# Kernel tuning notes

Measured on AMD Instinct MI355X. Metric: run time of the kernel, lower is better.

The kernel has to match this reference:

```python
import jax, jax.numpy as jnp
import numpy as np

N = 50176          # total nodes (128 alternating ligand/protein segments x 392 nodes)
SEGS = 128         # 2*B -> B = 64 complexes
PER = 392
E_BI = N * 4       # covalent-bond graph, avg degree 4
E_KNN = N * 16     # knn spatial graph, avg degree 16
F_IN = 64
D = 128            # f_bond = f_spatial
F_GATHER = 128
N_BOND_STEPS = 2
N_SPATIAL_STEPS = 2

def _lin(k, fi, fo):
    return jax.random.normal(k, (fi, fo), jnp.float32) / np.sqrt(fi)

def setup_inputs():
    ks = iter(jax.random.split(jax.random.key(0), 64))
    inp = {}
    inp["feat"] = jax.random.normal(next(ks), (N, F_IN), jnp.float32)
    inp["bi_src"] = jax.random.randint(next(ks), (E_BI,), 0, N)
    inp["bi_dst"] = jax.random.randint(next(ks), (E_BI,), 0, N)
    inp["bi_etype"] = jax.random.randint(next(ks), (E_BI,), 0, 5)
    inp["knn_src"] = jax.random.randint(next(ks), (E_KNN,), 0, N)
    inp["knn_dst"] = jax.random.randint(next(ks), (E_KNN,), 0, N)
    inp["knn_etype"] = jax.random.randint(next(ks), (E_KNN,), 0, 9)
    inp["batch_num_nodes"] = jnp.full((SEGS,), PER, jnp.int32)
    def gg(prefix, in_f, n_et):
        inp[prefix + "_W"] = jax.random.normal(next(ks), (n_et, D, D), jnp.float32) / np.sqrt(D)
        inp[prefix + "_b"] = jnp.zeros((n_et, D), jnp.float32)
        inp[prefix + "_wih"] = _lin(next(ks), D, 3 * D)
        inp[prefix + "_whh"] = _lin(next(ks), D, 3 * D)
        inp[prefix + "_bih"] = jnp.zeros((3 * D,), jnp.float32)
        inp[prefix + "_bhh"] = jnp.zeros((3 * D,), jnp.float32)
        inp[prefix + "_iw"] = _lin(next(ks), in_f + D, F_GATHER)
        inp[prefix + "_ib"] = jnp.zeros((F_GATHER,), jnp.float32)
        inp[prefix + "_jw"] = _lin(next(ks), D, F_GATHER)
        inp[prefix + "_jb"] = jnp.zeros((F_GATHER,), jnp.float32)
    gg("s1", F_IN, 5)
    gg("s2", F_GATHER, 9)
    inp["s3_w0"] = _lin(next(ks), F_GATHER, 256)
    inp["s3_b0"] = jnp.zeros((256,), jnp.float32)
    inp["s3_w1"] = _lin(next(ks), 256, 128)
    inp["s3_b1"] = jnp.zeros((128,), jnp.float32)
    inp["s3_wo"] = _lin(next(ks), 128, 1)
    inp["s3_bo"] = jnp.zeros((1,), jnp.float32)
    return inp

def _ggc(feat, src, dst, etype, W, b, wih, whh, bih, bhh, iw, ib, jw, jb, n_steps):
    n_nodes = feat.shape[0]
    n_et, d, _ = W.shape
    h = jnp.pad(feat, ((0, 0), (0, d - feat.shape[1])))  # zero_pad to out_feats
    def step(h, _):
        h_src = h[src]  # [E, d] gather
        m = jnp.zeros((src.shape[0], d), h.dtype)
        for i in range(n_et):  # per-edge-type linear, masked by one-hot edge type
            m = m + jnp.where((etype == i)[:, None], h_src @ W[i] + b[i], 0.0)
        a = jax.ops.segment_sum(m, dst, num_segments=n_nodes)  # scatter-sum (fn.sum)
        ir, iz, i_n = jnp.split(a @ wih + bih, 3, axis=-1)     # GRUCell, gate order r,z,n
        hr, hz, hn = jnp.split(h @ whh + bhh, 3, axis=-1)
        r = jax.nn.sigmoid(ir + hr)
        z = jax.nn.sigmoid(iz + hz)
        n = jnp.tanh(i_n + r * hn)
        return (1.0 - z) * n + z * h, None
    h, _ = jax.lax.scan(step, h, None, length=n_steps)
    # dropout is identity in eval mode
    return jax.nn.sigmoid(jnp.concatenate([h, feat], axis=1) @ iw + ib) * (h @ jw + jb)

def reference(feat, bi_src, bi_dst, bi_etype, knn_src, knn_dst, knn_etype, batch_num_nodes,
              s1_W, s1_b, s1_wih, s1_whh, s1_bih, s1_bhh, s1_iw, s1_ib, s1_jw, s1_jb,
              s2_W, s2_b, s2_wih, s2_whh, s2_bih, s2_bhh, s2_iw, s2_ib, s2_jw, s2_jb,
              s3_w0, s3_b0, s3_w1, s3_b1, s3_wo, s3_bo):
    h = _ggc(feat, bi_src, bi_dst, bi_etype, s1_W, s1_b, s1_wih, s1_whh, s1_bih, s1_bhh,
             s1_iw, s1_ib, s1_jw, s1_jb, N_BOND_STEPS)
    h = _ggc(h, knn_src, knn_dst, knn_etype, s2_W, s2_b, s2_wih, s2_whh, s2_bih, s2_bhh,
             s2_iw, s2_ib, s2_jw, s2_jb, N_SPATIAL_STEPS)
    segs = batch_num_nodes.shape[0]
    seg_id = jnp.repeat(jnp.arange(segs), batch_num_nodes, total_repeat_length=h.shape[0])
    pooled = jax.ops.segment_sum(h, seg_id, num_segments=segs)[0::2]  # ligand (even) segments
    x = jax.nn.relu(pooled @ s3_w0 + s3_b0)
    x = jax.nn.relu(x @ s3_w1 + s3_b1)
    return x @ s3_wo + s3_bo
```

## Files before the change

kernel.cpp:

```cpp
#include <hip/hip_runtime.h>
#include <hip/hip_bf16.h>

#define N_NODES 50176
#define PER 392
#define E_BI (N_NODES * 4)
#define E_KNN (N_NODES * 16)
#define E_TOT (E_BI + E_KNN)
#define KN_BI (N_NODES * 5)
#define KN_TOT (N_NODES * 14)
#define AH_S 416
#define AH_U 208

typedef __attribute__((ext_vector_type(8))) short short8;
typedef __attribute__((ext_vector_type(4))) float float4v;
typedef unsigned int uint;
typedef unsigned short ushort;

__device__ __forceinline__ float sigmoidf_(float x) { return 1.f / (1.f + __expf(-x)); }
__device__ __forceinline__ ushort f2bu(float x) {
    __hip_bfloat16 t = __float2bfloat16(x);
    return *reinterpret_cast<ushort*>(&t);
}
__device__ __forceinline__ float blo(uint u) { return __uint_as_float(u << 16); }
__device__ __forceinline__ float bhi(uint u) { return __uint_as_float(u & 0xFFFF0000u); }

__device__ __forceinline__ void gld_lds16(const ushort* g, ushort* l)
{
    __builtin_amdgcn_global_load_lds(
        (const __attribute__((address_space(1))) void*)g,
        (__attribute__((address_space(3))) void*)l, 16, 0, 0);
}

template<int NET>
__global__ __launch_bounds__(256) void msg_kernel(
    const uint* __restrict__ hb,
    const int* __restrict__ indptr,
    const int* __restrict__ elist,
    const ushort* __restrict__ Bfrag,
    ushort* __restrict__ aout)
{
    __shared__ ushort As[4][32][40];
    const int tid = threadIdx.x;
    const int bm = blockIdx.x * 32;
    const int wave = tid >> 6, lane = tid & 63;
    const int quad = lane >> 4, lrow = lane & 15;
    const int wr = wave & 1, wc = wave >> 1;
    const int r = tid >> 3;
    const int oct = tid & 7;
    const int v = bm + r;

    uint* AsU = (uint*)As;

    float4v acc[4] = {};

    for (int et = 0; et < NET; et++) {
        const int beg = indptr[v * NET + et], end = indptr[v * NET + et + 1];
        float av[16];
#pragma unroll
        for (int i = 0; i < 16; i++) av[i] = 0.f;

        for (int j = beg; j < end; j++) {
            int src = elist[j];
            const uint4* hp = (const uint4*)(hb + (size_t)src * 64 + oct * 8);
            uint4 u0 = hp[0];
            uint4 u1 = hp[1];
            av[0] += blo(u0.x); av[1] += bhi(u0.x);
            av[2] += blo(u0.y); av[3] += bhi(u0.y);
            av[4] += blo(u0.z); av[5] += bhi(u0.z);
            av[6] += blo(u0.w); av[7] += bhi(u0.w);
            av[8]  += blo(u1.x); av[9]  += bhi(u1.x);
            av[10] += blo(u1.y); av[11] += bhi(u1.y);
            av[12] += blo(u1.z); av[13] += bhi(u1.z);
            av[14] += blo(u1.w); av[15] += bhi(u1.w);
        }

        __syncthreads();
        {
            int base = ((oct >> 1) * 32 + r) * 20 + (oct & 1) * 8;
#pragma unroll
            for (int u = 0; u < 8; u++)
                AsU[base + u] = (uint)f2bu(av[2 * u]) | ((uint)f2bu(av[2 * u + 1]) << 16);
        }
        __syncthreads();

#pragma unroll
        for (int ch = 0; ch < 4; ch++) {
            short8 af = *(const short8*)&As[ch][wr * 16 + lrow][quad * 8];
            const ushort* bp = Bfrag + ((size_t)(((et * 4 + ch) * 2 + wc) * 4) << 9) + lane * 8;
#pragma unroll
            for (int j2 = 0; j2 < 4; j2++) {
                short8 bfr = *(const short8*)(bp + j2 * 512);
                acc[j2] = __builtin_amdgcn_mfma_f32_16x16x32_bf16(af, bfr, acc[j2], 0, 0, 0);
            }
        }
    }

#pragma unroll
    for (int j2 = 0; j2 < 4; j2++) {
        int col = wc * 64 + j2 * 16 + lrow;
#pragma unroll
        for (int rr = 0; rr < 4; rr++) {
            size_t row = (size_t)(bm + wr * 16 + quad * 4 + rr);
            aout[row * AH_S + col] = f2bu(acc[j2][rr]);
        }
    }
}

__global__ __launch_bounds__(256) void gru_gemm_kernel(
    const ushort* __restrict__ A,
    const ushort* __restrict__ Bt,
    const float* __restrict__ bias,
    ushort* __restrict__ ahOut, ushort* __restrict__ hbS)
{
    __shared__ ushort As[128 * 32];
    __shared__ ushort Bs[128 * 32];
    const int tid = threadIdx.x;
    const int bm = blockIdx.x * 128;
    const int bn = blockIdx.y * 128;
    const int wave = tid >> 6, lane = tid & 63;
    const int quad = lane >> 4, lrow = lane & 15;
    const int wr = wave & 1, wc = wave >> 1;

    float4v acc[4][4] = {};

    for (int k0 = 0; k0 < 288; k0 += 32) {
        __syncthreads();
#pragma unroll
        for (int p = 0; p < 2; p++) {
            int lin = p * 256 + tid;
            int r = lin >> 2;
            int kc = (lin & 3) * 8;
            int wb = (p * 256 + wave * 64) * 8;
            gld_lds16(A + (size_t)(bm + r) * AH_S + k0 + kc, &As[wb]);
            gld_lds16(Bt + (size_t)(bn + r) * 288 + k0 + kc, &Bs[wb]);
        }
        __syncthreads();
        short8 af[4], bfr[4];
#pragma unroll
        for (int i = 0; i < 4; i++)
            af[i] = *(const short8*)&As[(wr * 64 + i * 16 + lrow) * 32 + quad * 8];
#pragma unroll
        for (int j = 0; j < 4; j++)
            bfr[j] = *(const short8*)&Bs[(wc * 64 + j * 16 + lrow) * 32 + quad * 8];
#pragma unroll
        for (int i = 0; i < 4; i++)
#pragma unroll
            for (int j = 0; j < 4; j++)
                acc[i][j] = __builtin_amdgcn_mfma_f32_16x16x32_bf16(af[i], bfr[j], acc[i][j], 0, 0, 0);
    }

    const int ch = (bn >> 7) * 32 + wc * 16 + lrow;
    const float b0 = bias[bn + wc * 64 + lrow];
    const float b1 = bias[bn + wc * 64 + 16 + lrow];
    const float b2 = bias[bn + wc * 64 + 32 + lrow];
    const float b3 = bias[bn + wc * 64 + 48 + lrow];
#pragma unroll
    for (int i = 0; i < 4; i++) {
#pragma unroll
        for (int r = 0; r < 4; r++) {
            size_t row = (size_t)(bm + wr * 64 + i * 16 + quad * 4 + r);
            float rr = sigmoidf_(acc[i][0][r] + b0);
            float zz = sigmoidf_(acc[i][1][r] + b1);
            float nn = tanhf(acc[i][2][r] + b2 + rr * (acc[i][3][r] + b3));
            float hold = __uint_as_float(((uint)A[row * AH_S + 128 + ch]) << 16);
            float hnew = (1.f - zz) * nn + zz * hold;
            ushort hu = f2bu(hnew);
            ahOut[row * AH_S + 128 + ch] = hu;
            hbS[row * 128 + ch] = hu;
        }
    }
}

__global__ __launch_bounds__(256) void ro_gemm_kernel(
    const ushort* __restrict__ A,
    const ushort* __restrict__ Bt,
    const float* __restrict__ bias,
    ushort* __restrict__ rb)
{
    __shared__ ushort As[128 * 32];
    __shared__ ushort Bs[128 * 32];
    const int tid = threadIdx.x;
    const int bm = blockIdx.x * 128;
    const int bn = blockIdx.y * 128;
    const int wave = tid >> 6, lane = tid & 63;
    const int quad = lane >> 4, lrow = lane & 15;
    const int wr = wave & 1, wc = wave >> 1;

    float4v acc[4][4] = {};

    for (int k0 = 0; k0 < 288; k0 += 32) {
        __syncthreads();
#pragma unroll
        for (int p = 0; p < 2; p++) {
            int lin = p * 256 + tid;
            int r = lin >> 2;
            int kc = (lin & 3) * 8;
            int wb = (p * 256 + wave * 64) * 8;
            gld_lds16(A + (size_t)(bm + r) * AH_S + k0 + kc, &As[wb]);
            gld_lds16(Bt + (size_t)(bn + r) * 288 + k0 + kc, &Bs[wb]);
        }
        __syncthreads();
        short8 af[4], bfr[4];
#pragma unroll
        for (int i = 0; i < 4; i++)
            af[i] = *(const short8*)&As[(wr * 64 + i * 16 + lrow) * 32 + quad * 8];
#pragma unroll
        for (int j = 0; j < 4; j++)
            bfr[j] = *(const short8*)&Bs[(wc * 64 + j * 16 + lrow) * 32 + quad * 8];
#pragma unroll
        for (int i = 0; i < 4; i++)
#pragma unroll
            for (int j = 0; j < 4; j++)
                acc[i][j] = __builtin_amdgcn_mfma_f32_16x16x32_bf16(af[i], bfr[j], acc[i][j], 0, 0, 0);
    }

    const int c0 = (bn >> 7) * 64 + wc * 32 + lrow;
    const int c1 = c0 + 16;
    const float bu0 = bias[bn + wc * 64 + lrow];
    const float bv0 = bias[bn + wc * 64 + 16 + lrow];
    const float bu1 = bias[bn + wc * 64 + 32 + lrow];
    const float bv1 = bias[bn + wc * 64 + 48 + lrow];
#pragma unroll
    for (int i = 0; i < 4; i++) {
#pragma unroll
        for (int r = 0; r < 4; r++) {
            size_t row = (size_t)(bm + wr * 64 + i * 16 + quad * 4 + r);
            float o0 = sigmoidf_(acc[i][0][r] + bu0) * (acc[i][1][r] + bv0);
            float o1 = sigmoidf_(acc[i][2][r] + bu1) * (acc[i][3][r] + bv1);
            rb[row * 128 + c0] = f2bu(o0);
            rb[row * 128 + c1] = f2bu(o1);
        }
    }
}

__global__ __launch_bounds__(256) void gemm_kernel(
    const float* __restrict__ A, int lda,
    const float* __restrict__ B, int ldb,
    const float* __restrict__ bias,
    float* __restrict__ C, int ldc,
    int K, int act)
{
    __shared__ float As[32][68];
    __shared__ float Bs[32][68];
    const int tid = threadIdx.x;
    const int bm = blockIdx.x * 64;
    const int bn = blockIdx.y * 64;
    const int tm = (tid & 15) * 4;
    const int tn = (tid >> 4) * 4;
    float acc[4][4] = {};

    for (int k0 = 0; k0 < K; k0 += 32) {
#pragma unroll
        for (int p = 0; p < 2; p++) {
            int lin = p * 256 + tid;
            int ar = lin >> 3;
            int ac = (lin & 7) << 2;
            float4 av = *(const float4*)(A + (size_t)(bm + ar) * lda + (k0 + ac));
            As[ac + 0][ar] = av.x;
            As[ac + 1][ar] = av.y;
            As[ac + 2][ar] = av.z;
            As[ac + 3][ar] = av.w;
            int br = lin >> 4;
            int bc = (lin & 15) << 2;
            *(float4*)&Bs[br][bc] = *(const float4*)(B + (size_t)(k0 + br) * ldb + (bn + bc));
        }
        __syncthreads();
#pragma unroll
        for (int k = 0; k < 32; k++) {
            float4 a4 = *(const float4*)&As[k][tm];
            float4 b4 = *(const float4*)&Bs[k][tn];
            float av[4] = {a4.x, a4.y, a4.z, a4.w};
            float bv[4] = {b4.x, b4.y, b4.z, b4.w};
#pragma unroll
            for (int i = 0; i < 4; i++)
#pragma unroll
                for (int j = 0; j < 4; j++)
                    acc[i][j] += av[i] * bv[j];
        }
        __syncthreads();
    }
#pragma unroll
    for (int i = 0; i < 4; i++) {
        size_t row = (size_t)(bm + tm + i);
#pragma unroll
        for (int j = 0; j < 4; j++) {
            int col = bn + tn + j;
            float val = acc[i][j] + (bias ? bias[col] : 0.f);
            if (act == 1) val = fmaxf(val, 0.f);
            C[row * ldc + col] = val;
        }
    }
}

__global__ void prep_bfrag_kernel(const float* __restrict__ W, __hip_bfloat16* __restrict__ Bf,
                                  int net)
{
    int idx = blockIdx.x * blockDim.x + threadIdx.x;
    int m = idx & 7;
    int lane = (idx >> 3) & 63;
    int f = idx >> 9;
    int j = f & 3; f >>= 2;
    int wc = f & 1; f >>= 1;
    int ch = f & 3;
    int et = f >> 2;
    int quad = lane >> 4, lrow = lane & 15;
    int k = ch * 32 + quad * 8 + m;
    int c = wc * 64 + j * 16 + lrow;
    Bf[idx] = __float2bfloat16(W[et * 16384 + k * 128 + c]);
}

__global__ void prep_gru_kernel(const float* __restrict__ wih, const float* __restrict__ whh,
                                const float* __restrict__ bih, const float* __restrict__ bhh,
                                const float* __restrict__ b, int net,
                                __hip_bfloat16* __restrict__ Bt, float* __restrict__ bias)
{
    int idx = blockIdx.x * blockDim.x + threadIdx.x;
    int p = idx / 288;
    int k = idx - p * 288;
    int g = (p >> 4) & 3;
    int c = (p >> 7) * 32 + ((p >> 6) & 1) * 16 + (p & 15);
    float val = 0.f;
    if (k < 128) {
        if (g == 0)      val = wih[k * 384 + c];
        else if (g == 1) val = wih[k * 384 + 128 + c];
        else if (g == 2) val = wih[k * 384 + 256 + c];
    } else if (k < 256) {
        int kk = k - 128;
        if (g == 0)      val = whh[kk * 384 + c];
        else if (g == 1) val = whh[kk * 384 + 128 + c];
        else if (g == 3) val = whh[kk * 384 + 256 + c];
    } else {
        int j = k - 256;
        if (j < net && g < 3) {
            int col = g * 128 + c;
            float s = 0.f;
            for (int kk = 0; kk < 128; kk++) s += b[j * 128 + kk] * wih[kk * 384 + col];
            val = s;
        }
    }
    Bt[idx] = __float2bfloat16(val);
    if (k == 0) {
        float bv;
        if (g == 0)      bv = bih[c] + bhh[c];
        else if (g == 1) bv = bih[128 + c] + bhh[128 + c];
        else if (g == 2) bv = bih[256 + c];
        else             bv = bhh[256 + c];
        bias[p] = bv;
    }
}

__global__ void prep_ro_kernel(const float* __restrict__ iw, const float* __restrict__ jw,
                               const float* __restrict__ ib, const float* __restrict__ jb,
                               int Fin, __hip_bfloat16* __restrict__ Bt,
                               float* __restrict__ bias)
{
    int idx = blockIdx.x * blockDim.x + threadIdx.x;
    int p = idx / 288;
    int k = idx - p * 288;
    int j = (p >> 4) & 3;
    int s = j & 1;
    int c = ((p >> 7) & 1) * 64 + ((p >> 6) & 1) * 32 + (j >> 1) * 16 + (p & 15);
    float val = 0.f;
    if (k < 128) {
        val = s ? jw[k * 128 + c] : iw[k * 128 + c];
    } else if (k >= 160) {
        int kf = k - 160;
        if (kf < Fin && s == 0) val = iw[(128 + kf) * 128 + c];
    }
    Bt[idx] = __float2bfloat16(val);
    if (k == 0) bias[p] = s ? jb[c] : ib[c];
}

__global__ void hist2_kernel(const int* __restrict__ bd, const int* __restrict__ be,
                             const int* __restrict__ kd, const int* __restrict__ ke,
                             int* __restrict__ counts)
{
    int e = blockIdx.x * blockDim.x + threadIdx.x;
    if (e >= E_TOT) return;
    if (e < E_BI) atomicAdd(&counts[bd[e] * 5 + be[e]], 1);
    else { int i = e - E_BI; atomicAdd(&counts[KN_BI + kd[i] * 9 + ke[i]], 1); }
}

__global__ void scan1_kernel(const int* __restrict__ counts, int* __restrict__ local_ex,
                             int* __restrict__ partial)
{
    __shared__ int s[256];
    int t = threadIdx.x;
    int i = blockIdx.x * 256 + t;
    int v = counts[i];
    s[t] = v;
    __syncthreads();
    for (int off = 1; off < 256; off <<= 1) {
        int x = 0;
        if (t >= off) x = s[t - off];
        __syncthreads();
        if (t >= off) s[t] += x;
        __syncthreads();
    }
    local_ex[i] = s[t] - v;
    if (t == 255) partial[blockIdx.x] = s[255];
}

__global__ void scan2b_kernel(int* __restrict__ partial, int nb, int* __restrict__ last, int E)
{
    __shared__ int s[256];
    int t = threadIdx.x;
    int loc[11];
    int sum = 0;
#pragma unroll
    for (int q = 0; q < 11; q++) {
        int idx = t * 11 + q;
        int v = (idx < nb) ? partial[idx] : 0;
        loc[q] = sum; sum += v;
    }
    s[t] = sum;
    __syncthreads();
    for (int off = 1; off < 256; off <<= 1) {
        int x = 0;
        if (t >= off) x = s[t - off];
        __syncthreads();
        if (t >= off) s[t] += x;
        __syncthreads();
    }
    int excl = s[t] - sum;
#pragma unroll
    for (int q = 0; q < 11; q++) {
        int idx = t * 11 + q;
        if (idx < nb) partial[idx] = excl + loc[q];
    }
    if (t == 0) *last = E;
}

__global__ void scan3c_kernel(int* __restrict__ indptr, const int* __restrict__ partial,
                              int* __restrict__ cursor)
{
    int i = blockIdx.x * 256 + threadIdx.x;
    int v = indptr[i] + partial[blockIdx.x];
    indptr[i] = v;
    cursor[i] = v;
}

__global__ void fill2_kernel(const int* __restrict__ bs, const int* __restrict__ bd,
                             const int* __restrict__ be,
                             const int* __restrict__ ks, const int* __restrict__ kd,
                             const int* __restrict__ ke,
                             int* __restrict__ cursor, int* __restrict__ elist)
{
    int e = blockIdx.x * blockDim.x + threadIdx.x;
    if (e >= E_TOT) return;
    if (e < E_BI) {
        int pos = atomicAdd(&cursor[bd[e] * 5 + be[e]], 1);
        elist[pos] = bs[e];
    } else {
        int i = e - E_BI;
        int pos = atomicAdd(&cursor[KN_BI + kd[i] * 9 + ke[i]], 1);
        elist[pos] = ks[i];
    }
}

__global__ void pad_cnt_kernel(const float* __restrict__ fsrc, const ushort* __restrict__ bsrc,
                               const int* __restrict__ indptr, int net,
                               uint* __restrict__ ahA, uint* __restrict__ ahB,
                               uint* __restrict__ hb, int Fin)
{
    int idx = blockIdx.x * blockDim.x + threadIdx.x;
    int v = idx >> 5;
    int j = idx & 31;
    int c = j * 4;
    float4 val = make_float4(0.f, 0.f, 0.f, 0.f);
    if (bsrc) {
        uint2 u = *(const uint2*)(bsrc + (size_t)v * Fin + c);
        val.x = blo(u.x); val.y = bhi(u.x);
        val.z = blo(u.y); val.w = bhi(u.y);
    } else if (c < Fin) {
        val = *(const float4*)(fsrc + (size_t)v * Fin + c);
    }
    uint2 pk;
    pk.x = (uint)f2bu(val.x) | ((uint)f2bu(val.y) << 16);
    pk.y = (uint)f2bu(val.z) | ((uint)f2bu(val.w) << 16);
    *(uint2*)(ahA + (size_t)v * AH_U + 64 + c / 2) = pk;
    *(uint2*)(ahA + (size_t)v * AH_U + 144 + c / 2) = pk;
    *(uint2*)(ahB + (size_t)v * AH_U + 144 + c / 2) = pk;
    *(uint2*)(hb + (size_t)v * 64 + c / 2) = pk;
    float cv = 0.f;
    if (j < net) cv = (float)(indptr[v * net + j + 1] - indptr[v * net + j]);
    ushort u = f2bu(cv);
    ((ushort*)ahA)[(size_t)v * AH_S + 256 + j] = u;
    ((ushort*)ahB)[(size_t)v * AH_S + 256 + j] = u;
}

__global__ void pool_kernel(const ushort* __restrict__ r2, float* __restrict__ pooled)
{
    int s = blockIdx.x;
    int c = threadIdx.x;
    const ushort* base = r2 + (size_t)(2 * s) * PER * 128;
    float acc = 0.f;
    for (int i = 0; i < PER; i++)
        acc += __uint_as_float(((uint)base[(size_t)i * 128 + c]) << 16);
    pooled[s * 128 + c] = acc;
}

__global__ void out_kernel(const float* __restrict__ x2, const float* __restrict__ wo,
                           const float* __restrict__ bo, float* __restrict__ out)
{
    int row = blockIdx.x;
    int t = threadIdx.x;
    float s = x2[row * 128 + t] * wo[t] + x2[row * 128 + 64 + t] * wo[64 + t];
#pragma unroll
    for (int off = 32; off; off >>= 1) s += __shfl_down(s, off);
    if (t == 0) out[row] = s + bo[0];
}

struct GGParams {
    const float *W, *b, *wih, *whh, *bih, *bhh, *iw, *ib, *jw, *jb;
};

struct WsPtrs {
    __hip_bfloat16 *ah0, *ah1;
    float* G;
    uint* hb;
    __hip_bfloat16* r1b;
    __hip_bfloat16 *bfragB, *gruB, *roB;
    float *gruBias, *roBias;
    int *indptr, *cursor, *partial, *elist;
    float *pooled, *x1, *x2;
};

template<int NET>
static void run_stage(hipStream_t st, const float* featF, const __hip_bfloat16* featB, int Fin,
                      const GGParams& p, const WsPtrs& w, const int* indptr_slice,
                      __hip_bfloat16* rout_b)
{
    const int N = N_NODES;
    ushort* ahA = (ushort*)w.ah0;
    ushort* ahB = (ushort*)w.ah1;
    ushort* hbS = (ushort*)w.hb;

    prep_bfrag_kernel<<<(NET * 16384) / 256, 256, 0, st>>>(p.W, w.bfragB, NET);
    prep_gru_kernel<<<(512 * 288) / 256, 256, 0, st>>>(p.wih, p.whh, p.bih, p.bhh, p.b, NET,
                                                       w.gruB, w.gruBias);
    prep_ro_kernel<<<(256 * 288) / 256, 256, 0, st>>>(p.iw, p.jw, p.ib, p.jb, Fin,
                                                      w.roB, w.roBias);

    pad_cnt_kernel<<<(N * 32) / 256, 256, 0, st>>>(featF, (const ushort*)featB,
                                                   indptr_slice, NET,
                                                   (uint*)ahA, (uint*)ahB, w.hb, Fin);

    ushort* ahIn = ahA;
    ushort* ahOut = ahB;
    for (int step = 0; step < 2; step++) {
        msg_kernel<NET><<<N / 32, 256, 0, st>>>(w.hb, indptr_slice, w.elist,
                                                (ushort*)w.bfragB, ahIn);
        dim3 g(N / 128, 4);
        gru_gemm_kernel<<<g, 256, 0, st>>>(ahIn, (ushort*)w.gruB, w.gruBias, ahOut, hbS);
        ushort* t = ahIn; ahIn = ahOut; ahOut = t;
    }
    dim3 gr(N / 128, 2);
    ro_gemm_kernel<<<gr, 256, 0, st>>>(ahIn + 128, (ushort*)w.roB, w.roBias,
                                       (ushort*)rout_b);
}

extern "C" void kernel_launch(void* const* d_in, const int* in_sizes, int n_in,
                              void* d_out, int out_size, void* d_ws, size_t ws_size,
                              hipStream_t stream)
{
    const float* feat    = (const float*)d_in[0];
    const int*   bi_src  = (const int*)d_in[1];
    const int*   bi_dst  = (const int*)d_in[2];
    const int*   bi_et   = (const int*)d_in[3];
    const int*   knn_src = (const int*)d_in[4];
    const int*   knn_dst = (const int*)d_in[5];
    const int*   knn_et  = (const int*)d_in[6];

    GGParams s1 { (const float*)d_in[8],  (const float*)d_in[9],  (const float*)d_in[10],
                  (const float*)d_in[11], (const float*)d_in[12], (const float*)d_in[13],
                  (const float*)d_in[14], (const float*)d_in[15], (const float*)d_in[16],
                  (const float*)d_in[17] };
    GGParams s2 { (const float*)d_in[18], (const float*)d_in[19], (const float*)d_in[20],
                  (const float*)d_in[21], (const float*)d_in[22], (const float*)d_in[23],
                  (const float*)d_in[24], (const float*)d_in[25], (const float*)d_in[26],
                  (const float*)d_in[27] };
    const float* w0 = (const float*)d_in[28];
    const float* b0 = (const float*)d_in[29];
    const float* w1 = (const float*)d_in[30];
    const float* b1 = (const float*)d_in[31];
    const float* wo = (const float*)d_in[32];
    const float* bo = (const float*)d_in[33];

    const int N = N_NODES;
    const size_t n128 = (size_t)N * 128;

    float* ws = (float*)d_ws;
    WsPtrs w;
    size_t off = 0;
    w.ah0    = (__hip_bfloat16*)(ws + off);    off += (size_t)N * 208;
    w.ah1    = (__hip_bfloat16*)(ws + off);    off += (size_t)N * 208;
    w.G      = ws + off;                       off += 2 * n128;
    w.hb     = (uint*)(w.G + n128);
    w.r1b    = (__hip_bfloat16*)(ws + off);    off += n128 / 2;
    w.bfragB = (__hip_bfloat16*)(ws + off);    off += 9 * 16384 / 2;
    w.gruB   = (__hip_bfloat16*)(ws + off);    off += 512 * 288 / 2;
    w.roB    = (__hip_bfloat16*)(ws + off);    off += 256 * 288 / 2;
    w.gruBias = ws + off;                      off += 512;
    w.roBias  = ws + off;                      off += 256;
    w.indptr  = (int*)(ws + off);              off += KN_TOT + 8;
    w.cursor  = (int*)(ws + off);              off += KN_TOT;
    w.partial = (int*)(ws + off);              off += 4096;
    w.elist   = (int*)(ws + off);              off += E_TOT;
    w.pooled  = ws + off;                      off += 64 * 128;
    w.x1      = ws + off;                      off += 64 * 256;
    w.x2      = ws + off;                      off += 64 * 128;

    hipMemsetAsync(w.cursor, 0, KN_TOT * sizeof(int), stream);
    hist2_kernel<<<(E_TOT + 255) / 256, 256, 0, stream>>>(bi_dst, bi_et, knn_dst, knn_et, w.cursor);
    scan1_kernel<<<KN_TOT / 256, 256, 0, stream>>>(w.cursor, w.indptr, w.partial);
    scan2b_kernel<<<1, 256, 0, stream>>>(w.partial, KN_TOT / 256, w.indptr + KN_TOT, E_TOT);
    scan3c_kernel<<<KN_TOT / 256, 256, 0, stream>>>(w.indptr, w.partial, w.cursor);
    fill2_kernel<<<(E_TOT + 255) / 256, 256, 0, stream>>>(bi_src, bi_dst, bi_et,
                                                          knn_src, knn_dst, knn_et,
                                                          w.cursor, w.elist);

    run_stage<5>(stream, feat, nullptr, 64, s1, w, w.indptr, w.r1b);
    __hip_bfloat16* r2b = (__hip_bfloat16*)w.G;
    run_stage<9>(stream, nullptr, w.r1b, 128, s2, w, w.indptr + KN_BI, r2b);

    pool_kernel<<<64, 128, 0, stream>>>((const ushort*)r2b, w.pooled);
    {
        dim3 g1(1, 4);
        gemm_kernel<<<g1, 256, 0, stream>>>(w.pooled, 128, w0, 256, b0, w.x1, 256, 128, 1);
        dim3 g2(1, 2);
        gemm_kernel<<<g2, 256, 0, stream>>>(w.x1, 256, w1, 128, b1, w.x2, 128, 256, 1);
    }
    out_kernel<<<64, 64, 0, stream>>>(w.x2, wo, bo, (float*)d_out);
}
```

Measured before the change: 725.1 us.

## Fuse stage-1 readout into stage-2 input layout and merge prep and MLP kernels

The stage-1 readout GEMM now writes its output straight into the stage-2 padded activation buffer and the bf16 hidden-state buffer. This removes the separate r1b round trip and the bf16-to-padded copy in pad_cnt, leaving a small cnt_kernel to fill only the edge-type count columns. All weight-prep kernels for both stages are merged into one launch. The last two MLP layers and the output dot product are merged into one kernel, which cuts launch count at the cost of a single-block serial tail kernel.

```diff
diff --git a/kernel.cpp b/kernel.cpp
--- a/kernel.cpp
+++ b/kernel.cpp
@@ -175,7 +175,8 @@
     const ushort* __restrict__ A,
     const ushort* __restrict__ Bt,
     const float* __restrict__ bias,
-    ushort* __restrict__ rb)
+    ushort* __restrict__ rb,
+    ushort* __restrict__ ahx, ushort* __restrict__ hbS)
 {
     __shared__ ushort As[128 * 32];
     __shared__ ushort Bs[128 * 32];
@@ -227,8 +228,19 @@
             size_t row = (size_t)(bm + wr * 64 + i * 16 + quad * 4 + r);
             float o0 = sigmoidf_(acc[i][0][r] + bu0) * (acc[i][1][r] + bv0);
             float o1 = sigmoidf_(acc[i][2][r] + bu1) * (acc[i][3][r] + bv1);
-            rb[row * 128 + c0] = f2bu(o0);
-            rb[row * 128 + c1] = f2bu(o1);
+            ushort u0 = f2bu(o0), u1 = f2bu(o1);
+            if (rb) {
+                rb[row * 128 + c0] = u0;
+                rb[row * 128 + c1] = u1;
+            }
+            if (ahx) {
+                ahx[row * AH_S + 128 + c0] = u0;
+                ahx[row * AH_S + 128 + c1] = u1;
+                ahx[row * AH_S + 288 + c0] = u0;
+                ahx[row * AH_S + 288 + c1] = u1;
+                hbS[row * 128 + c0] = u0;
+                hbS[row * 128 + c1] = u1;
+            }
         }
     }
 }
@@ -292,10 +304,38 @@
     }
 }
 
-__global__ void prep_bfrag_kernel(const float* __restrict__ W, __hip_bfloat16* __restrict__ Bf,
-                                  int net)
-{
-    int idx = blockIdx.x * blockDim.x + threadIdx.x;
+__global__ __launch_bounds__(256) void mlp2_kernel(
+    const float* __restrict__ x1, const float* __restrict__ w1,
+    const float* __restrict__ b1, const float* __restrict__ wo,
+    const float* __restrict__ bo, float* __restrict__ out)
+{
+    __shared__ float part[256];
+    int t = threadIdx.x;
+    int row = t >> 2;
+    int pq = t & 3;
+    float acc[32];
+#pragma unroll
+    for (int i = 0; i < 32; i++) acc[i] = 0.f;
+    const float* xr = x1 + row * 256;
+    for (int k = 0; k < 256; k++) {
+        float xv = xr[k];
+        const float* wr = w1 + k * 128 + pq * 32;
+#pragma unroll
+        for (int i = 0; i < 32; i++) acc[i] += xv * wr[i];
+    }
+    float s = 0.f;
+#pragma unroll
+    for (int i = 0; i < 32; i++) {
+        float v = fmaxf(acc[i] + b1[pq * 32 + i], 0.f);
+        s += v * wo[pq * 32 + i];
+    }
+    part[t] = s;
+    __syncthreads();
+    if (pq == 0) out[row] = part[t] + part[t + 1] + part[t + 2] + part[t + 3] + bo[0];
+}
+
+__device__ __forceinline__ void prep_bfrag_item(const float* W, ushort* Bf, int idx)
+{
     int m = idx & 7;
     int lane = (idx >> 3) & 63;
     int f = idx >> 9;
@@ -306,15 +346,14 @@
     int quad = lane >> 4, lrow = lane & 15;
     int k = ch * 32 + quad * 8 + m;
     int c = wc * 64 + j * 16 + lrow;
-    Bf[idx] = __float2bfloat16(W[et * 16384 + k * 128 + c]);
-}
-
-__global__ void prep_gru_kernel(const float* __restrict__ wih, const float* __restrict__ whh,
-                                const float* __restrict__ bih, const float* __restrict__ bhh,
-                                const float* __restrict__ b, int net,
-                                __hip_bfloat16* __restrict__ Bt, float* __restrict__ bias)
-{
-    int idx = blockIdx.x * blockDim.x + threadIdx.x;
+    Bf[idx] = f2bu(W[et * 16384 + k * 128 + c]);
+}
+
+__device__ __forceinline__ void prep_gru_item(const float* wih, const float* whh,
+                                              const float* bih, const float* bhh,
+                                              const float* b, int net,
+                                              ushort* Bt, float* bias, int idx)
+{
     int p = idx / 288;
     int k = idx - p * 288;
     int g = (p >> 4) & 3;
@@ -338,7 +377,7 @@
             val = s;
         }
     }
-    Bt[idx] = __float2bfloat16(val);
+    Bt[idx] = f2bu(val);
     if (k == 0) {
         float bv;
         if (g == 0)      bv = bih[c] + bhh[c];
@@ -349,12 +388,10 @@
     }
 }
 
-__global__ void prep_ro_kernel(const float* __restrict__ iw, const float* __restrict__ jw,
-                               const float* __restrict__ ib, const float* __restrict__ jb,
-                               int Fin, __hip_bfloat16* __restrict__ Bt,
-                               float* __restrict__ bias)
-{
-    int idx = blockIdx.x * blockDim.x + threadIdx.x;
+__device__ __forceinline__ void prep_ro_item(const float* iw, const float* jw,
+                                             const float* ib, const float* jb,
+                                             int Fin, ushort* Bt, float* bias, int idx)
+{
     int p = idx / 288;
     int k = idx - p * 288;
     int j = (p >> 4) & 3;
@@ -367,8 +404,27 @@
         int kf = k - 160;
         if (kf < Fin && s == 0) val = iw[(128 + kf) * 128 + c];
     }
-    Bt[idx] = __float2bfloat16(val);
+    Bt[idx] = f2bu(val);
     if (k == 0) bias[p] = s ? jb[c] : ib[c];
+}
+
+__global__ __launch_bounds__(256) void prep_all_kernel(
+    const float* W1, const float* b1, const float* wih1, const float* whh1,
+    const float* bih1, const float* bhh1, const float* iw1, const float* ib1,
+    const float* jw1, const float* jb1,
+    const float* W2, const float* b2, const float* wih2, const float* whh2,
+    const float* bih2, const float* bhh2, const float* iw2, const float* ib2,
+    const float* jw2, const float* jb2,
+    ushort* bf1, ushort* gru1, float* gb1, ushort* ro1, float* rb1,
+    ushort* bf2, ushort* gru2, float* gb2, ushort* ro2, float* rb2)
+{
+    int gid = blockIdx.x * 256 + threadIdx.x;
+    if (gid < 81920)            prep_bfrag_item(W1, bf1, gid);
+    else if (gid < 229376)      prep_gru_item(wih1, whh1, bih1, bhh1, b1, 5, gru1, gb1, gid - 81920);
+    else if (gid < 303104)      prep_ro_item(iw1, jw1, ib1, jb1, 64, ro1, rb1, gid - 229376);
+    else if (gid < 450560)      prep_bfrag_item(W2, bf2, gid - 303104);
+    else if (gid < 598016)      prep_gru_item(wih2, whh2, bih2, bhh2, b2, 9, gru2, gb2, gid - 450560);
+    else                        prep_ro_item(iw2, jw2, ib2, jb2, 128, ro2, rb2, gid - 598016);
 }
 
 __global__ void hist2_kernel(const int* __restrict__ bd, const int* __restrict__ be,
@@ -458,7 +514,7 @@
     }
 }
 
-__global__ void pad_cnt_kernel(const float* __restrict__ fsrc, const ushort* __restrict__ bsrc,
+__global__ void pad_cnt_kernel(const float* __restrict__ fsrc,
                                const int* __restrict__ indptr, int net,
                                uint* __restrict__ ahA, uint* __restrict__ ahB,
                                uint* __restrict__ hb, int Fin)
@@ -468,13 +524,7 @@
     int j = idx & 31;
     int c = j * 4;
     float4 val = make_float4(0.f, 0.f, 0.f, 0.f);
-    if (bsrc) {
-        uint2 u = *(const uint2*)(bsrc + (size_t)v * Fin + c);
-        val.x = blo(u.x); val.y = bhi(u.x);
-        val.z = blo(u.y); val.w = bhi(u.y);
-    } else if (c < Fin) {
-        val = *(const float4*)(fsrc + (size_t)v * Fin + c);
-    }
+    if (c < Fin) val = *(const float4*)(fsrc + (size_t)v * Fin + c);
     uint2 pk;
     pk.x = (uint)f2bu(val.x) | ((uint)f2bu(val.y) << 16);
     pk.y = (uint)f2bu(val.z) | ((uint)f2bu(val.w) << 16);
@@ -489,6 +539,19 @@
     ((ushort*)ahB)[(size_t)v * AH_S + 256 + j] = u;
 }
 
+__global__ void cnt_kernel(const int* __restrict__ indptr, int net,
+                           ushort* __restrict__ ahA, ushort* __restrict__ ahB)
+{
+    int idx = blockIdx.x * blockDim.x + threadIdx.x;
+    int v = idx >> 5;
+    int j = idx & 31;
+    float cv = 0.f;
+    if (j < net) cv = (float)(indptr[v * net + j + 1] - indptr[v * net + j]);
+    ushort u = f2bu(cv);
+    ahA[(size_t)v * AH_S + 256 + j] = u;
+    ahB[(size_t)v * AH_S + 256 + j] = u;
+}
+
 __global__ void pool_kernel(const ushort* __restrict__ r2, float* __restrict__ pooled)
 {
     int s = blockIdx.x;
@@ -500,65 +563,9 @@
     pooled[s * 128 + c] = acc;
 }
 
-__global__ void out_kernel(const float* __restrict__ x2, const float* __restrict__ wo,
-                           const float* __restrict__ bo, float* __restrict__ out)
-{
-    int row = blockIdx.x;
-    int t = threadIdx.x;
-    float s = x2[row * 128 + t] * wo[t] + x2[row * 128 + 64 + t] * wo[64 + t];
-#pragma unroll
-    for (int off = 32; off; off >>= 1) s += __shfl_down(s, off);
-    if (t == 0) out[row] = s + bo[0];
-}
-
 struct GGParams {
     const float *W, *b, *wih, *whh, *bih, *bhh, *iw, *ib, *jw, *jb;
 };
-
-struct WsPtrs {
-    __hip_bfloat16 *ah0, *ah1;
-    float* G;
-    uint* hb;
-    __hip_bfloat16* r1b;
-    __hip_bfloat16 *bfragB, *gruB, *roB;
-    float *gruBias, *roBias;
-    int *indptr, *cursor, *partial, *elist;
-    float *pooled, *x1, *x2;
-};
-
-template<int NET>
-static void run_stage(hipStream_t st, const float* featF, const __hip_bfloat16* featB, int Fin,
-                      const GGParams& p, const WsPtrs& w, const int* indptr_slice,
-                      __hip_bfloat16* rout_b)
-{
-    const int N = N_NODES;
-    ushort* ahA = (ushort*)w.ah0;
-    ushort* ahB = (ushort*)w.ah1;
-    ushort* hbS = (ushort*)w.hb;
-
-    prep_bfrag_kernel<<<(NET * 16384) / 256, 256, 0, st>>>(p.W, w.bfragB, NET);
-    prep_gru_kernel<<<(512 * 288) / 256, 256, 0, st>>>(p.wih, p.whh, p.bih, p.bhh, p.b, NET,
-                                                       w.gruB, w.gruBias);
-    prep_ro_kernel<<<(256 * 288) / 256, 256, 0, st>>>(p.iw, p.jw, p.ib, p.jb, Fin,
-                                                      w.roB, w.roBias);
-
-    pad_cnt_kernel<<<(N * 32) / 256, 256, 0, st>>>(featF, (const ushort*)featB,
-                                                   indptr_slice, NET,
-                                                   (uint*)ahA, (uint*)ahB, w.hb, Fin);
-
-    ushort* ahIn = ahA;
-    ushort* ahOut = ahB;
-    for (int step = 0; step < 2; step++) {
-        msg_kernel<NET><<<N / 32, 256, 0, st>>>(w.hb, indptr_slice, w.elist,
-                                                (ushort*)w.bfragB, ahIn);
-        dim3 g(N / 128, 4);
-        gru_gemm_kernel<<<g, 256, 0, st>>>(ahIn, (ushort*)w.gruB, w.gruBias, ahOut, hbS);
-        ushort* t = ahIn; ahIn = ahOut; ahOut = t;
-    }
-    dim3 gr(N / 128, 2);
-    ro_gemm_kernel<<<gr, 256, 0, st>>>(ahIn + 128, (ushort*)w.roB, w.roBias,
-                                       (ushort*)rout_b);
-}
 
 extern "C" void kernel_launch(void* const* d_in, const int* in_sizes, int n_in,
                               void* d_out, int out_size, void* d_ws, size_t ws_size,
@@ -591,45 +598,83 @@
     const size_t n128 = (size_t)N * 128;
 
     float* ws = (float*)d_ws;
-    WsPtrs w;
     size_t off = 0;
-    w.ah0    = (__hip_bfloat16*)(ws + off);    off += (size_t)N * 208;
-    w.ah1    = (__hip_bfloat16*)(ws + off);    off += (size_t)N * 208;
-    w.G      = ws + off;                       off += 2 * n128;
-    w.hb     = (uint*)(w.G + n128);
-    w.r1b    = (__hip_bfloat16*)(ws + off);    off += n128 / 2;
-    w.bfragB = (__hip_bfloat16*)(ws + off);    off += 9 * 16384 / 2;
-    w.gruB   = (__hip_bfloat16*)(ws + off);    off += 512 * 288 / 2;
-    w.roB    = (__hip_bfloat16*)(ws + off);    off += 256 * 288 / 2;
-    w.gruBias = ws + off;                      off += 512;
-    w.roBias  = ws + off;                      off += 256;
-    w.indptr  = (int*)(ws + off);              off += KN_TOT + 8;
-    w.cursor  = (int*)(ws + off);              off += KN_TOT;
-    w.partial = (int*)(ws + off);              off += 4096;
-    w.elist   = (int*)(ws + off);              off += E_TOT;
-    w.pooled  = ws + off;                      off += 64 * 128;
-    w.x1      = ws + off;                      off += 64 * 256;
-    w.x2      = ws + off;                      off += 64 * 128;
-
-    hipMemsetAsync(w.cursor, 0, KN_TOT * sizeof(int), stream);
-    hist2_kernel<<<(E_TOT + 255) / 256, 256, 0, stream>>>(bi_dst, bi_et, knn_dst, knn_et, w.cursor);
-    scan1_kernel<<<KN_TOT / 256, 256, 0, stream>>>(w.cursor, w.indptr, w.partial);
-    scan2b_kernel<<<1, 256, 0, stream>>>(w.partial, KN_TOT / 256, w.indptr + KN_TOT, E_TOT);
-    scan3c_kernel<<<KN_TOT / 256, 256, 0, stream>>>(w.indptr, w.partial, w.cursor);
+    __hip_bfloat16* ah0 = (__hip_bfloat16*)(ws + off);  off += (size_t)N * 208;
+    __hip_bfloat16* ah1 = (__hip_bfloat16*)(ws + off);  off += (size_t)N * 208;
+    float* G = ws + off;                                off += 2 * n128;
+    uint* hb = (uint*)(G + n128);
+    ushort* bfragB1 = (ushort*)(ws + off);              off += 81920 / 2;
+    ushort* bfragB2 = (ushort*)(ws + off);              off += 147456 / 2;
+    ushort* gruB1 = (ushort*)(ws + off);                off += 147456 / 2;
+    ushort* gruB2 = (ushort*)(ws + off);                off += 147456 / 2;
+    ushort* roB1 = (ushort*)(ws + off);                 off += 73728 / 2;
+    ushort* roB2 = (ushort*)(ws + off);                 off += 73728 / 2;
+    float* gruBias1 = ws + off;                         off += 512;
+    float* gruBias2 = ws + off;                         off += 512;
+    float* roBias1 = ws + off;                          off += 256;
+    float* roBias2 = ws + off;                          off += 256;
+    int* indptr  = (int*)(ws + off);                    off += KN_TOT + 8;
+    int* cursor  = (int*)(ws + off);                    off += KN_TOT;
+    int* partial = (int*)(ws + off);                    off += 4096;
+    int* elist   = (int*)(ws + off);                    off += E_TOT;
+    float* pooled = ws + off;                           off += 64 * 128;
+    float* x1 = ws + off;                               off += 64 * 256;
+
+    ushort* ahA = (ushort*)ah0;
+    ushort* ahB = (ushort*)ah1;
+    ushort* hbS = (ushort*)hb;
+
+    prep_all_kernel<<<2624, 256, 0, stream>>>(
+        s1.W, s1.b, s1.wih, s1.whh, s1.bih, s1.bhh, s1.iw, s1.ib, s1.jw, s1.jb,
+        s2.W, s2.b, s2.wih, s2.whh, s2.bih, s2.bhh, s2.iw, s2.ib, s2.jw, s2.jb,
+        bfragB1, gruB1, gruBias1, roB1, roBias1,
+        bfragB2, gruB2, gruBias2, roB2, roBias2);
+
+    hipMemsetAsync(cursor, 0, KN_TOT * sizeof(int), stream);
+    hist2_kernel<<<(E_TOT + 255) / 256, 256, 0, stream>>>(bi_dst, bi_et, knn_dst, knn_et, cursor);
+    scan1_kernel<<<KN_TOT / 256, 256, 0, stream>>>(cursor, indptr, partial);
+    scan2b_kernel<<<1, 256, 0, stream>>>(partial, KN_TOT / 256, indptr + KN_TOT, E_TOT);
+    scan3c_kernel<<<KN_TOT / 256, 256, 0, stream>>>(indptr, partial, cursor);
     fill2_kernel<<<(E_TOT + 255) / 256, 256, 0, stream>>>(bi_src, bi_dst, bi_et,
                                                           knn_src, knn_dst, knn_et,
-                                                          w.cursor, w.elist);
-
-    run_stage<5>(stream, feat, nullptr, 64, s1, w, w.indptr, w.r1b);
-    __hip_bfloat16* r2b = (__hip_bfloat16*)w.G;
-    run_stage<9>(stream, nullptr, w.r1b, 128, s2, w, w.indptr + KN_BI, r2b);
-
-    pool_kernel<<<64, 128, 0, stream>>>((const ushort*)r2b, w.pooled);
+                                                          cursor, elist);
+
+    pad_cnt_kernel<<<(N * 32) / 256, 256, 0, stream>>>(feat, indptr, 5,
+                                                       (uint*)ahA, (uint*)ahB, hb, 64);
+    {
+        ushort* ahIn = ahA;
+        ushort* ahOut = ahB;
+        for (int step = 0; step < 2; step++) {
+            msg_kernel<5><<<N / 32, 256, 0, stream>>>(hb, indptr, elist, bfragB1, ahIn);
+            dim3 g(N / 128, 4);
+            gru_gemm_kernel<<<g, 256, 0, stream>>>(ahIn, gruB1, gruBias1, ahOut, hbS);
+            ushort* t = ahIn; ahIn = ahOut; ahOut = t;
+        }
+        dim3 gr(N / 128, 2);
+        ro_gemm_kernel<<<gr, 256, 0, stream>>>(ahIn + 128, roB1, roBias1,
+                                               nullptr, ahB, hbS);
+    }
+
+    cnt_kernel<<<(N * 32) / 256, 256, 0, stream>>>(indptr + KN_BI, 9, ahA, ahB);
+    __hip_bfloat16* r2b = (__hip_bfloat16*)G;
+    {
+        ushort* ahIn = ahB;
+        ushort* ahOut = ahA;
+        for (int step = 0; step < 2; step++) {
+            msg_kernel<9><<<N / 32, 256, 0, stream>>>(hb, indptr + KN_BI, elist, bfragB2, ahIn);
+            dim3 g(N / 128, 4);
+            gru_gemm_kernel<<<g, 256, 0, stream>>>(ahIn, gruB2, gruBias2, ahOut, hbS);
+            ushort* t = ahIn; ahIn = ahOut; ahOut = t;
+        }
+        dim3 gr(N / 128, 2);
+        ro_gemm_kernel<<<gr, 256, 0, stream>>>(ahIn + 128, roB2, roBias2,
+                                               (ushort*)r2b, nullptr, nullptr);
+    }
+
+    pool_kernel<<<64, 128, 0, stream>>>((const ushort*)r2b, pooled);
     {
         dim3 g1(1, 4);
-        gemm_kernel<<<g1, 256, 0, stream>>>(w.pooled, 128, w0, 256, b0, w.x1, 256, 128, 1);
-        dim3 g2(1, 2);
-        gemm_kernel<<<g2, 256, 0, stream>>>(w.x1, 256, w1, 128, b1, w.x2, 128, 256, 1);
-    }
-    out_kernel<<<64, 64, 0, stream>>>(w.x2, wo, bo, (float*)d_out);
-}
+        gemm_kernel<<<g1, 256, 0, stream>>>(pooled, 128, w0, 256, b0, x1, 256, 128, 1);
+    }
+    mlp2_kernel<<<1, 256, 0, stream>>>(x1, w1, b1, wo, bo, (float*)d_out);
+}
```

Measured after the change: 929.6 us. 28.2% more time.
